# Kernel tuning notes

Hardware: AMD Instinct MI355X
Metric: run time of the kernel (lower is better)

The kernel has to match this reference:

```python
import jax, jax.numpy as jnp
import numpy as np

N_NODES = 50000
N_EDGES = 500000
D_NODE = 64
D_EDGE = 32
MSG_DIM = 2 * D_NODE + D_EDGE      # 160
HID_DIM = MSG_DIM + D_NODE         # 224
ALPHA = 0.01                       # LeakyReLU slope


def setup_inputs() -> dict:
    key = jax.random.key(0)
    ks = jax.random.split(key, 8)
    h_n = jax.random.normal(ks[0], (N_NODES, D_NODE), dtype=jnp.float32)
    h_e = jax.random.normal(ks[1], (N_EDGES, D_EDGE), dtype=jnp.float32)
    src = jax.random.randint(ks[2], (N_EDGES,), 0, N_NODES, dtype=jnp.int32)
    dst = jax.random.randint(ks[3], (N_EDGES,), 0, N_NODES, dtype=jnp.int32)
    W_msg = jax.random.normal(ks[4], (MSG_DIM, MSG_DIM), dtype=jnp.float32) * 0.05
    b_msg = jax.random.normal(ks[5], (MSG_DIM,), dtype=jnp.float32) * 0.05
    W_hid = jax.random.normal(ks[6], (HID_DIM, HID_DIM), dtype=jnp.float32) * 0.05
    b_hid = jax.random.normal(ks[7], (HID_DIM,), dtype=jnp.float32) * 0.05
    return {"h_n": h_n, "h_e": h_e, "src": src, "dst": dst,
            "W_msg": W_msg, "b_msg": b_msg, "W_hid": W_hid, "b_hid": b_hid}


def reference(h_n, h_e, src, dst, W_msg, b_msg, W_hid, b_hid):
    # --- message: gather src/dst node features + edge features, linear + leaky_relu ---
    m_input = jnp.concatenate([h_n[src], h_n[dst], h_e], axis=-1)   # [E, MSG_DIM]
    m = jax.nn.leaky_relu(m_input @ W_msg.T + b_msg, negative_slope=ALPHA)
    # --- reduce: sum messages at destination nodes (DGL fn.sum) ---
    m_sum = jax.ops.segment_sum(m, dst, num_segments=N_NODES)       # [N, MSG_DIM]
    # --- update: concat(m_sum, h_n), linear + leaky_relu ---
    h_input = jnp.concatenate([m_sum, h_n], axis=-1)                # [N, HID_DIM]
    h_out = jax.nn.leaky_relu(h_input @ W_hid.T + b_hid, negative_slope=ALPHA)
    # single graph with unique node ids: split/squeeze is identity
    return h_out
```

## Files before the change

kernel.cpp:

```cpp
#include <hip/hip_runtime.h>

#define N_NODES 50000
#define N_EDGES 500000
#define D_NODE 64
#define D_EDGE 32
#define MSG_DIM 160
#define HID_DIM 224
#define ALPHA 0.01f

#define FNB 16
#define NBKT 3125
#define BKT_CAP 256
#define A_STRIDE 168
#define MT_STRIDE 72
#define CURSOR_PAD 16
#define CVT_BLKS 3200
#define SCAT_BLKS 1954

typedef unsigned short u16;
typedef unsigned long long u64;
typedef short short8 __attribute__((ext_vector_type(8)));
typedef float float4v __attribute__((ext_vector_type(4)));

static __device__ __forceinline__ u16 f2bf(float f) {
    unsigned int u = __float_as_uint(f);
    u += 0x7fffu + ((u >> 16) & 1u);
    return (u16)(u >> 16);
}

__global__ __launch_bounds__(256) void cvt_scatter(const float* __restrict__ h_n,
                                                   const float* __restrict__ W_msg,
                                                   const float* __restrict__ W_hid,
                                                   const int* __restrict__ src,
                                                   const int* __restrict__ dst,
                                                   u16* __restrict__ hn_bf,
                                                   u16* __restrict__ Wm_bf,
                                                   u16* __restrict__ Wh_bf,
                                                   int* __restrict__ cursor,
                                                   u64* __restrict__ pack) {
    const int b = blockIdx.x;
    if (b < CVT_BLKS) {
        int i = b * 256 + threadIdx.x;
        const float* in; u16* outp; int j;
        if (i < 800000)      { in = h_n;   outp = hn_bf; j = i; }
        else if (i < 806400) { in = W_msg; outp = Wm_bf; j = i - 800000; }
        else if (i < 818944) { in = W_hid; outp = Wh_bf; j = i - 806400; }
        else return;
        float4 v = reinterpret_cast<const float4*>(in)[j];
        ushort4 o;
        o.x = f2bf(v.x); o.y = f2bf(v.y); o.z = f2bf(v.z); o.w = f2bf(v.w);
        reinterpret_cast<ushort4*>(outp)[j] = o;
    } else {
        int e = (b - CVT_BLKS) * 256 + threadIdx.x;
        if (e < N_EDGES) {
            int d = dst[e];
            int bk = d >> 4;
            int idx = atomicAdd(&cursor[bk * CURSOR_PAD], 1);
            if (idx < BKT_CAP)
                pack[(size_t)bk * BKT_CAP + idx] =
                    ((u64)e << 34) | ((u64)d << 17) | (u64)src[e];
        }
    }
}

__global__ __launch_bounds__(256) void fused_kernel(
    const u16* __restrict__ hn_bf, const float* __restrict__ h_e,
    const u64* __restrict__ pack, const int* __restrict__ cursor,
    const u16* __restrict__ Wm_bf, const float* __restrict__ b_msg,
    const u16* __restrict__ Wh_bf, const float* __restrict__ b_hid,
    float* __restrict__ out)
{
    __shared__ alignas(16) u16 X_lds[64 * A_STRIDE];
    __shared__ alignas(16) u16 MT[4 * 16 * MT_STRIDE];
    __shared__ alignas(16) u16 dst16[64];

    const int tid = threadIdx.x;
    const int n0 = blockIdx.x * FNB;
    const int p_begin = blockIdx.x * BKT_CAP;
    int ecnt = cursor[blockIdx.x * CURSOR_PAD];
    if (ecnt > BKT_CAP) ecnt = BKT_CAP;
    const int p_end = p_begin + ecnt;

    const int wave = tid >> 6, lane = tid & 63;
    const int qd = lane >> 4, l15 = lane & 15;
    const int e_loc = tid >> 2, j4 = tid & 3;

    const int nchunk = (wave < 2) ? 3 : 2;
    float biasv[3];
#pragma unroll
    for (int ci = 0; ci < 3; ++ci) {
        const int c = wave + ci * 4;
        biasv[ci] = (c < 10) ? b_msg[c * 16 + l15] : 0.f;
    }
    float4v m_acc[3] = {{0,0,0,0},{0,0,0,0},{0,0,0,0}};
    u16* MTw = &MT[wave * 16 * MT_STRIDE];

    u64 pk_cur = 0, pk_nxt = 0;
    uint4 sA, sB, dA, dB;
    float4 heA, heB;
    if (p_begin < p_end) {
        int pp = p_begin + e_loc;
        int pidx = (pp < p_end) ? pp : (p_end - 1);
        pk_cur = pack[pidx];
        const int s  = (int)(pk_cur & 0x1FFFF);
        const int d  = (int)((pk_cur >> 17) & 0x1FFFF);
        const int eo = (int)(pk_cur >> 34);
        const uint4* srow = reinterpret_cast<const uint4*>(hn_bf + (size_t)s * D_NODE);
        const uint4* drow = reinterpret_cast<const uint4*>(hn_bf + (size_t)d * D_NODE);
        sA = srow[j4 * 2]; sB = srow[j4 * 2 + 1];
        dA = drow[j4 * 2]; dB = drow[j4 * 2 + 1];
        const float4* he = reinterpret_cast<const float4*>(h_e + (size_t)eo * D_EDGE);
        heA = he[j4 * 2]; heB = he[j4 * 2 + 1];
        int pp1 = pp + 64;
        pk_nxt = pack[(pp1 < p_end) ? pp1 : (p_end - 1)];
    }

    for (int p0 = p_begin; p0 < p_end; p0 += 64) {
        {
            const bool padE = (p0 + e_loc >= p_end);
            const int d = (int)((pk_cur >> 17) & 0x1FFFF);
            if (j4 == 0) dst16[e_loc] = padE ? (u16)0xFFFFu : (u16)(d - n0);
            uint4* Arow = reinterpret_cast<uint4*>(&X_lds[e_loc * A_STRIDE]);
            Arow[j4 * 2]     = sA;
            Arow[j4 * 2 + 1] = sB;
            Arow[8 + j4 * 2]     = dA;
            Arow[8 + j4 * 2 + 1] = dB;
            ushort4 lo, hi;
            lo.x = f2bf(heA.x); lo.y = f2bf(heA.y); lo.z = f2bf(heA.z); lo.w = f2bf(heA.w);
            hi.x = f2bf(heB.x); hi.y = f2bf(heB.y); hi.z = f2bf(heB.z); hi.w = f2bf(heB.w);
            ushort4* Aus = reinterpret_cast<ushort4*>(Arow);
            Aus[32 + j4 * 2]     = lo;
            Aus[32 + j4 * 2 + 1] = hi;
        }
        __syncthreads();

        short8 xf[4][5];
#pragma unroll
        for (int s = 0; s < 4; ++s)
#pragma unroll
            for (int ks = 0; ks < 5; ++ks)
                xf[s][ks] = *reinterpret_cast<const short8*>(
                    &X_lds[(s * 16 + l15) * A_STRIDE + ks * 32 + qd * 8]);

        short8 a2[2];
#pragma unroll
        for (int fi = 0; fi < 2; ++fi) {
            short8 dv = *reinterpret_cast<const short8*>(&dst16[fi * 32 + qd * 8]);
            short8 t;
#pragma unroll
            for (int j = 0; j < 8; ++j)
                t[j] = (short)(((int)(u16)dv[j] == l15) ? 0x3F80 : 0);
            a2[fi] = t;
        }

        if (p0 + 64 < p_end) {
            pk_cur = pk_nxt;
            const int s  = (int)(pk_cur & 0x1FFFF);
            const int eo = (int)(pk_cur >> 34);
            const int d  = (int)((pk_cur >> 17) & 0x1FFFF);
            const uint4* srow = reinterpret_cast<const uint4*>(hn_bf + (size_t)s * D_NODE);
            const uint4* drow = reinterpret_cast<const uint4*>(hn_bf + (size_t)d * D_NODE);
            sA = srow[j4 * 2]; sB = srow[j4 * 2 + 1];
            dA = drow[j4 * 2]; dB = drow[j4 * 2 + 1];
            const float4* he = reinterpret_cast<const float4*>(h_e + (size_t)eo * D_EDGE);
            heA = he[j4 * 2]; heB = he[j4 * 2 + 1];
            int pp2 = p0 + 128 + e_loc;
            pk_nxt = pack[(pp2 < p_end) ? pp2 : (p_end - 1)];
        }
        __syncthreads();

        for (int ci = 0; ci < nchunk; ++ci) {
            const int c = wave + ci * 4;
            const int fbase = c * 16;
            short8 wf[5];
#pragma unroll
            for (int ks = 0; ks < 5; ++ks)
                wf[ks] = *reinterpret_cast<const short8*>(
                    Wm_bf + (size_t)(fbase + l15) * MSG_DIM + ks * 32 + qd * 8);
            const float bias = biasv[ci];
#pragma unroll
            for (int s = 0; s < 4; ++s) {
                float4v acc = {0.f, 0.f, 0.f, 0.f};
#pragma unroll
                for (int ks = 0; ks < 5; ++ks)
                    acc = __builtin_amdgcn_mfma_f32_16x16x32_bf16(xf[s][ks], wf[ks], acc, 0, 0, 0);
                float v0 = acc[0] + bias, v1 = acc[1] + bias,
                      v2 = acc[2] + bias, v3 = acc[3] + bias;
                v0 = fmaxf(v0, ALPHA * v0); v1 = fmaxf(v1, ALPHA * v1);
                v2 = fmaxf(v2, ALPHA * v2); v3 = fmaxf(v3, ALPHA * v3);
                ushort4 m4;
                m4.x = f2bf(v0); m4.y = f2bf(v1); m4.z = f2bf(v2); m4.w = f2bf(v3);
                *reinterpret_cast<ushort4*>(&MTw[l15 * MT_STRIDE + s * 16 + qd * 4]) = m4;
            }
            short8 b2_0 = *reinterpret_cast<const short8*>(&MTw[l15 * MT_STRIDE + qd * 8]);
            short8 b2_1 = *reinterpret_cast<const short8*>(&MTw[l15 * MT_STRIDE + 32 + qd * 8]);
            m_acc[ci] = __builtin_amdgcn_mfma_f32_16x16x32_bf16(a2[0], b2_0, m_acc[ci], 0, 0, 0);
            m_acc[ci] = __builtin_amdgcn_mfma_f32_16x16x32_bf16(a2[1], b2_1, m_acc[ci], 0, 0, 0);
        }
    }
    __syncthreads();

    u16* Xb = X_lds;
    for (int ci = 0; ci < nchunk; ++ci) {
        const int c = wave + ci * 4;
#pragma unroll
        for (int r = 0; r < 4; ++r)
            Xb[(qd * 4 + r) * A_STRIDE + c * 16 + l15] = f2bf(m_acc[ci][r]);
    }
    __syncthreads();

    const int node = n0 + l15;
    short8 b_frag[7];
#pragma unroll
    for (int ks = 0; ks < 5; ++ks)
        b_frag[ks] = *reinterpret_cast<const short8*>(
            &Xb[l15 * A_STRIDE + ks * 32 + qd * 8]);
#pragma unroll
    for (int ks = 5; ks < 7; ++ks)
        b_frag[ks] = *reinterpret_cast<const short8*>(
            hn_bf + (size_t)node * D_NODE + (ks - 5) * 32 + qd * 8);

    for (int c = wave; c < 14; c += 4) {
        float4v acc = {0.f, 0.f, 0.f, 0.f};
#pragma unroll
        for (int ks = 0; ks < 7; ++ks) {
            short8 a = *reinterpret_cast<const short8*>(
                Wh_bf + (size_t)(c * 16 + l15) * HID_DIM + ks * 32 + qd * 8);
            acc = __builtin_amdgcn_mfma_f32_16x16x32_bf16(a, b_frag[ks], acc, 0, 0, 0);
        }
        const float4 bias = *reinterpret_cast<const float4*>(b_hid + c * 16 + qd * 4);
        float v0 = acc[0] + bias.x, v1 = acc[1] + bias.y,
              v2 = acc[2] + bias.z, v3 = acc[3] + bias.w;
        v0 = fmaxf(v0, ALPHA * v0); v1 = fmaxf(v1, ALPHA * v1);
        v2 = fmaxf(v2, ALPHA * v2); v3 = fmaxf(v3, ALPHA * v3);
        float4 o; o.x = v0; o.y = v1; o.z = v2; o.w = v3;
        *reinterpret_cast<float4*>(&out[(size_t)node * HID_DIM + c * 16 + qd * 4]) = o;
    }
}

extern "C" void kernel_launch(void* const* d_in, const int* in_sizes, int n_in,
                              void* d_out, int out_size, void* d_ws, size_t ws_size,
                              hipStream_t stream)
{
    const float* h_n   = (const float*)d_in[0];
    const float* h_e   = (const float*)d_in[1];
    const int*   src   = (const int*)d_in[2];
    const int*   dst   = (const int*)d_in[3];
    const float* W_msg = (const float*)d_in[4];
    const float* b_msg = (const float*)d_in[5];
    const float* W_hid = (const float*)d_in[6];
    const float* b_hid = (const float*)d_in[7];
    float* out = (float*)d_out;

    char* ws = (char*)d_ws;
    u16* hn_bf  = (u16*)(ws + 0);
    u16* Wm_bf  = (u16*)(ws + 6400000);
    u16* Wh_bf  = (u16*)(ws + 6451200);
    int* cursor = (int*)(ws + 6551552);
    u64* pack   = (u64*)(ws + 6751552);

    hipMemsetAsync(cursor, 0, (size_t)NBKT * CURSOR_PAD * sizeof(int), stream);
    cvt_scatter<<<CVT_BLKS + SCAT_BLKS, 256, 0, stream>>>(
        h_n, W_msg, W_hid, src, dst, hn_bf, Wm_bf, Wh_bf, cursor, pack);
    fused_kernel<<<NBKT, 256, 0, stream>>>(
        hn_bf, h_e, pack, cursor, Wm_bf, b_msg, Wh_bf, b_hid, out);
}
```

Measured before the change: 271.8 us.

## Load MFMA edge fragments directly from global memory, drop LDS staging

```diff
diff --git a/kernel.cpp b/kernel.cpp
--- a/kernel.cpp
+++ b/kernel.cpp
@@ -11,7 +11,7 @@
 #define FNB 16
 #define NBKT 3125
 #define BKT_CAP 256
-#define A_STRIDE 168
+#define XB_STRIDE 168
 #define MT_STRIDE 72
 #define CURSOR_PAD 16
 #define CVT_BLKS 3200
@@ -63,27 +63,25 @@
     }
 }
 
-__global__ __launch_bounds__(256) void fused_kernel(
+__global__ __launch_bounds__(256, 4) void fused_kernel(
     const u16* __restrict__ hn_bf, const float* __restrict__ h_e,
     const u64* __restrict__ pack, const int* __restrict__ cursor,
     const u16* __restrict__ Wm_bf, const float* __restrict__ b_msg,
     const u16* __restrict__ Wh_bf, const float* __restrict__ b_hid,
     float* __restrict__ out)
 {
-    __shared__ alignas(16) u16 X_lds[64 * A_STRIDE];
     __shared__ alignas(16) u16 MT[4 * 16 * MT_STRIDE];
-    __shared__ alignas(16) u16 dst16[64];
+    __shared__ alignas(16) u16 Xb[FNB * XB_STRIDE];
 
     const int tid = threadIdx.x;
     const int n0 = blockIdx.x * FNB;
     const int p_begin = blockIdx.x * BKT_CAP;
     int ecnt = cursor[blockIdx.x * CURSOR_PAD];
     if (ecnt > BKT_CAP) ecnt = BKT_CAP;
-    const int p_end = p_begin + ecnt;
 
     const int wave = tid >> 6, lane = tid & 63;
     const int qd = lane >> 4, l15 = lane & 15;
-    const int e_loc = tid >> 2, j4 = tid & 3;
+    const int myrow = n0 + l15;
 
     const int nchunk = (wave < 2) ? 3 : 2;
     float biasv[3];
@@ -95,79 +93,50 @@
     float4v m_acc[3] = {{0,0,0,0},{0,0,0,0},{0,0,0,0}};
     u16* MTw = &MT[wave * 16 * MT_STRIDE];
 
-    u64 pk_cur = 0, pk_nxt = 0;
-    uint4 sA, sB, dA, dB;
-    float4 heA, heB;
-    if (p_begin < p_end) {
-        int pp = p_begin + e_loc;
-        int pidx = (pp < p_end) ? pp : (p_end - 1);
-        pk_cur = pack[pidx];
-        const int s  = (int)(pk_cur & 0x1FFFF);
-        const int d  = (int)((pk_cur >> 17) & 0x1FFFF);
-        const int eo = (int)(pk_cur >> 34);
-        const uint4* srow = reinterpret_cast<const uint4*>(hn_bf + (size_t)s * D_NODE);
-        const uint4* drow = reinterpret_cast<const uint4*>(hn_bf + (size_t)d * D_NODE);
-        sA = srow[j4 * 2]; sB = srow[j4 * 2 + 1];
-        dA = drow[j4 * 2]; dB = drow[j4 * 2 + 1];
-        const float4* he = reinterpret_cast<const float4*>(h_e + (size_t)eo * D_EDGE);
-        heA = he[j4 * 2]; heB = he[j4 * 2 + 1];
-        int pp1 = pp + 64;
-        pk_nxt = pack[(pp1 < p_end) ? pp1 : (p_end - 1)];
-    }
-
-    for (int p0 = p_begin; p0 < p_end; p0 += 64) {
-        {
-            const bool padE = (p0 + e_loc >= p_end);
-            const int d = (int)((pk_cur >> 17) & 0x1FFFF);
-            if (j4 == 0) dst16[e_loc] = padE ? (u16)0xFFFFu : (u16)(d - n0);
-            uint4* Arow = reinterpret_cast<uint4*>(&X_lds[e_loc * A_STRIDE]);
-            Arow[j4 * 2]     = sA;
-            Arow[j4 * 2 + 1] = sB;
-            Arow[8 + j4 * 2]     = dA;
-            Arow[8 + j4 * 2 + 1] = dB;
-            ushort4 lo, hi;
-            lo.x = f2bf(heA.x); lo.y = f2bf(heA.y); lo.z = f2bf(heA.z); lo.w = f2bf(heA.w);
-            hi.x = f2bf(heB.x); hi.y = f2bf(heB.y); hi.z = f2bf(heB.z); hi.w = f2bf(heB.w);
-            ushort4* Aus = reinterpret_cast<ushort4*>(Arow);
-            Aus[32 + j4 * 2]     = lo;
-            Aus[32 + j4 * 2 + 1] = hi;
-        }
-        __syncthreads();
-
+    for (int p0 = 0; p0 < ecnt; p0 += 64) {
         short8 xf[4][5];
 #pragma unroll
-        for (int s = 0; s < 4; ++s)
-#pragma unroll
-            for (int ks = 0; ks < 5; ++ks)
-                xf[s][ks] = *reinterpret_cast<const short8*>(
-                    &X_lds[(s * 16 + l15) * A_STRIDE + ks * 32 + qd * 8]);
+        for (int s = 0; s < 4; ++s) {
+            int x = p0 + s * 16 + l15;
+            if (x > ecnt - 1) x = ecnt - 1;
+            const u64 pk = pack[p_begin + x];
+            const int sr = (int)(pk & 0x1FFFF);
+            const int dr = (int)((pk >> 17) & 0x1FFFF);
+            const int eo = (int)(pk >> 34);
+            const short8* srow = reinterpret_cast<const short8*>(
+                hn_bf + (size_t)sr * D_NODE + qd * 8);
+            xf[s][0] = srow[0];
+            xf[s][1] = srow[4];
+            const short8* drow = reinterpret_cast<const short8*>(
+                hn_bf + (size_t)dr * D_NODE + qd * 8);
+            xf[s][2] = drow[0];
+            xf[s][3] = drow[4];
+            const float4* he = reinterpret_cast<const float4*>(
+                h_e + (size_t)eo * D_EDGE + qd * 8);
+            float4 ha = he[0], hb = he[1];
+            short8 t;
+            t[0] = (short)f2bf(ha.x); t[1] = (short)f2bf(ha.y);
+            t[2] = (short)f2bf(ha.z); t[3] = (short)f2bf(ha.w);
+            t[4] = (short)f2bf(hb.x); t[5] = (short)f2bf(hb.y);
+            t[6] = (short)f2bf(hb.z); t[7] = (short)f2bf(hb.w);
+            xf[s][4] = t;
+        }
 
         short8 a2[2];
 #pragma unroll
         for (int fi = 0; fi < 2; ++fi) {
-            short8 dv = *reinterpret_cast<const short8*>(&dst16[fi * 32 + qd * 8]);
+            const int xb = p0 + fi * 32 + qd * 8;
+            const u64* pb = pack + p_begin + xb;
+            const int nv = ecnt - xb;
             short8 t;
 #pragma unroll
-            for (int j = 0; j < 8; ++j)
-                t[j] = (short)(((int)(u16)dv[j] == l15) ? 0x3F80 : 0);
+            for (int j = 0; j < 8; ++j) {
+                const u64 pk = pb[j];
+                const int dr = (int)((pk >> 17) & 0x1FFFF);
+                t[j] = (short)((j < nv && dr == myrow) ? 0x3F80 : 0);
+            }
             a2[fi] = t;
         }
-
-        if (p0 + 64 < p_end) {
-            pk_cur = pk_nxt;
-            const int s  = (int)(pk_cur & 0x1FFFF);
-            const int eo = (int)(pk_cur >> 34);
-            const int d  = (int)((pk_cur >> 17) & 0x1FFFF);
-            const uint4* srow = reinterpret_cast<const uint4*>(hn_bf + (size_t)s * D_NODE);
-            const uint4* drow = reinterpret_cast<const uint4*>(hn_bf + (size_t)d * D_NODE);
-            sA = srow[j4 * 2]; sB = srow[j4 * 2 + 1];
-            dA = drow[j4 * 2]; dB = drow[j4 * 2 + 1];
-            const float4* he = reinterpret_cast<const float4*>(h_e + (size_t)eo * D_EDGE);
-            heA = he[j4 * 2]; heB = he[j4 * 2 + 1];
-            int pp2 = p0 + 128 + e_loc;
-            pk_nxt = pack[(pp2 < p_end) ? pp2 : (p_end - 1)];
-        }
-        __syncthreads();
 
         for (int ci = 0; ci < nchunk; ++ci) {
             const int c = wave + ci * 4;
@@ -198,14 +167,12 @@
             m_acc[ci] = __builtin_amdgcn_mfma_f32_16x16x32_bf16(a2[1], b2_1, m_acc[ci], 0, 0, 0);
         }
     }
-    __syncthreads();
-
-    u16* Xb = X_lds;
+
     for (int ci = 0; ci < nchunk; ++ci) {
         const int c = wave + ci * 4;
 #pragma unroll
         for (int r = 0; r < 4; ++r)
-            Xb[(qd * 4 + r) * A_STRIDE + c * 16 + l15] = f2bf(m_acc[ci][r]);
+            Xb[(qd * 4 + r) * XB_STRIDE + c * 16 + l15] = f2bf(m_acc[ci][r]);
     }
     __syncthreads();
 
@@ -214,7 +181,7 @@
 #pragma unroll
     for (int ks = 0; ks < 5; ++ks)
         b_frag[ks] = *reinterpret_cast<const short8*>(
-            &Xb[l15 * A_STRIDE + ks * 32 + qd * 8]);
+            &Xb[l15 * XB_STRIDE + ks * 32 + qd * 8]);
 #pragma unroll
     for (int ks = 5; ks < 7; ++ks)
         b_frag[ks] = *reinterpret_cast<const short8*>(
```

New measurement: 380.9 us. 40.1% more time.

## Merge memset, convert/scatter, and fused compute into one cooperative persistent kernel

Applied to the files above, without the earlier changes.

```diff
diff --git a/kernel.cpp b/kernel.cpp
--- a/kernel.cpp
+++ b/kernel.cpp
@@ -1,4 +1,7 @@
 #include <hip/hip_runtime.h>
+#include <hip/hip_cooperative_groups.h>
+
+namespace cg = cooperative_groups;
 
 #define N_NODES 50000
 #define N_EDGES 500000
@@ -14,8 +17,7 @@
 #define A_STRIDE 168
 #define MT_STRIDE 72
 #define CURSOR_PAD 16
-#define CVT_BLKS 3200
-#define SCAT_BLKS 1954
+#define CVT_N 818944
 
 typedef unsigned short u16;
 typedef unsigned long long u64;
@@ -28,59 +30,47 @@
     return (u16)(u >> 16);
 }
 
-__global__ __launch_bounds__(256) void cvt_scatter(const float* __restrict__ h_n,
-                                                   const float* __restrict__ W_msg,
-                                                   const float* __restrict__ W_hid,
-                                                   const int* __restrict__ src,
-                                                   const int* __restrict__ dst,
-                                                   u16* __restrict__ hn_bf,
-                                                   u16* __restrict__ Wm_bf,
-                                                   u16* __restrict__ Wh_bf,
-                                                   int* __restrict__ cursor,
-                                                   u64* __restrict__ pack) {
-    const int b = blockIdx.x;
-    if (b < CVT_BLKS) {
-        int i = b * 256 + threadIdx.x;
+__global__ __launch_bounds__(256, 4) void mega_kernel(
+    const float* __restrict__ h_n, const float* __restrict__ h_e,
+    const int* __restrict__ src, const int* __restrict__ dst,
+    const float* __restrict__ W_msg, const float* __restrict__ b_msg,
+    const float* __restrict__ W_hid, const float* __restrict__ b_hid,
+    u16* __restrict__ hn_bf, u16* __restrict__ Wm_bf, u16* __restrict__ Wh_bf,
+    int* __restrict__ cursor, u64* __restrict__ pack,
+    float* __restrict__ out)
+{
+    cg::grid_group grid = cg::this_grid();
+    const int tid  = threadIdx.x;
+    const int gtid = blockIdx.x * 256 + tid;
+    const int gstr = gridDim.x * 256;
+
+    for (int i = gtid; i < NBKT * CURSOR_PAD; i += gstr) cursor[i] = 0;
+    grid.sync();
+
+    for (int i = gtid; i < CVT_N; i += gstr) {
         const float* in; u16* outp; int j;
         if (i < 800000)      { in = h_n;   outp = hn_bf; j = i; }
         else if (i < 806400) { in = W_msg; outp = Wm_bf; j = i - 800000; }
-        else if (i < 818944) { in = W_hid; outp = Wh_bf; j = i - 806400; }
-        else return;
+        else                 { in = W_hid; outp = Wh_bf; j = i - 806400; }
         float4 v = reinterpret_cast<const float4*>(in)[j];
         ushort4 o;
         o.x = f2bf(v.x); o.y = f2bf(v.y); o.z = f2bf(v.z); o.w = f2bf(v.w);
         reinterpret_cast<ushort4*>(outp)[j] = o;
-    } else {
-        int e = (b - CVT_BLKS) * 256 + threadIdx.x;
-        if (e < N_EDGES) {
-            int d = dst[e];
-            int bk = d >> 4;
-            int idx = atomicAdd(&cursor[bk * CURSOR_PAD], 1);
-            if (idx < BKT_CAP)
-                pack[(size_t)bk * BKT_CAP + idx] =
-                    ((u64)e << 34) | ((u64)d << 17) | (u64)src[e];
-        }
-    }
-}
-
-__global__ __launch_bounds__(256) void fused_kernel(
-    const u16* __restrict__ hn_bf, const float* __restrict__ h_e,
-    const u64* __restrict__ pack, const int* __restrict__ cursor,
-    const u16* __restrict__ Wm_bf, const float* __restrict__ b_msg,
-    const u16* __restrict__ Wh_bf, const float* __restrict__ b_hid,
-    float* __restrict__ out)
-{
+    }
+    for (int e = gtid; e < N_EDGES; e += gstr) {
+        int d = dst[e];
+        int bk = d >> 4;
+        int idx = atomicAdd(&cursor[bk * CURSOR_PAD], 1);
+        if (idx < BKT_CAP)
+            pack[(size_t)bk * BKT_CAP + idx] =
+                ((u64)e << 34) | ((u64)d << 17) | (u64)src[e];
+    }
+    grid.sync();
+
     __shared__ alignas(16) u16 X_lds[64 * A_STRIDE];
     __shared__ alignas(16) u16 MT[4 * 16 * MT_STRIDE];
     __shared__ alignas(16) u16 dst16[64];
 
-    const int tid = threadIdx.x;
-    const int n0 = blockIdx.x * FNB;
-    const int p_begin = blockIdx.x * BKT_CAP;
-    int ecnt = cursor[blockIdx.x * CURSOR_PAD];
-    if (ecnt > BKT_CAP) ecnt = BKT_CAP;
-    const int p_end = p_begin + ecnt;
-
     const int wave = tid >> 6, lane = tid & 63;
     const int qd = lane >> 4, l15 = lane & 15;
     const int e_loc = tid >> 2, j4 = tid & 3;
@@ -92,149 +82,159 @@
         const int c = wave + ci * 4;
         biasv[ci] = (c < 10) ? b_msg[c * 16 + l15] : 0.f;
     }
-    float4v m_acc[3] = {{0,0,0,0},{0,0,0,0},{0,0,0,0}};
     u16* MTw = &MT[wave * 16 * MT_STRIDE];
 
-    u64 pk_cur = 0, pk_nxt = 0;
-    uint4 sA, sB, dA, dB;
-    float4 heA, heB;
-    if (p_begin < p_end) {
-        int pp = p_begin + e_loc;
-        int pidx = (pp < p_end) ? pp : (p_end - 1);
-        pk_cur = pack[pidx];
-        const int s  = (int)(pk_cur & 0x1FFFF);
-        const int d  = (int)((pk_cur >> 17) & 0x1FFFF);
-        const int eo = (int)(pk_cur >> 34);
-        const uint4* srow = reinterpret_cast<const uint4*>(hn_bf + (size_t)s * D_NODE);
-        const uint4* drow = reinterpret_cast<const uint4*>(hn_bf + (size_t)d * D_NODE);
-        sA = srow[j4 * 2]; sB = srow[j4 * 2 + 1];
-        dA = drow[j4 * 2]; dB = drow[j4 * 2 + 1];
-        const float4* he = reinterpret_cast<const float4*>(h_e + (size_t)eo * D_EDGE);
-        heA = he[j4 * 2]; heB = he[j4 * 2 + 1];
-        int pp1 = pp + 64;
-        pk_nxt = pack[(pp1 < p_end) ? pp1 : (p_end - 1)];
-    }
-
-    for (int p0 = p_begin; p0 < p_end; p0 += 64) {
-        {
-            const bool padE = (p0 + e_loc >= p_end);
-            const int d = (int)((pk_cur >> 17) & 0x1FFFF);
-            if (j4 == 0) dst16[e_loc] = padE ? (u16)0xFFFFu : (u16)(d - n0);
-            uint4* Arow = reinterpret_cast<uint4*>(&X_lds[e_loc * A_STRIDE]);
-            Arow[j4 * 2]     = sA;
-            Arow[j4 * 2 + 1] = sB;
-            Arow[8 + j4 * 2]     = dA;
-            Arow[8 + j4 * 2 + 1] = dB;
-            ushort4 lo, hi;
-            lo.x = f2bf(heA.x); lo.y = f2bf(heA.y); lo.z = f2bf(heA.z); lo.w = f2bf(heA.w);
-            hi.x = f2bf(heB.x); hi.y = f2bf(heB.y); hi.z = f2bf(heB.z); hi.w = f2bf(heB.w);
-            ushort4* Aus = reinterpret_cast<ushort4*>(Arow);
-            Aus[32 + j4 * 2]     = lo;
-            Aus[32 + j4 * 2 + 1] = hi;
-        }
-        __syncthreads();
-
-        short8 xf[4][5];
-#pragma unroll
-        for (int s = 0; s < 4; ++s)
-#pragma unroll
-            for (int ks = 0; ks < 5; ++ks)
-                xf[s][ks] = *reinterpret_cast<const short8*>(
-                    &X_lds[(s * 16 + l15) * A_STRIDE + ks * 32 + qd * 8]);
-
-        short8 a2[2];
-#pragma unroll
-        for (int fi = 0; fi < 2; ++fi) {
-            short8 dv = *reinterpret_cast<const short8*>(&dst16[fi * 32 + qd * 8]);
-            short8 t;
-#pragma unroll
-            for (int j = 0; j < 8; ++j)
-                t[j] = (short)(((int)(u16)dv[j] == l15) ? 0x3F80 : 0);
-            a2[fi] = t;
-        }
-
-        if (p0 + 64 < p_end) {
-            pk_cur = pk_nxt;
+    for (int bk = blockIdx.x; bk < NBKT; bk += gridDim.x) {
+        const int n0 = bk * FNB;
+        const int p_begin = bk * BKT_CAP;
+        int ecnt = cursor[bk * CURSOR_PAD];
+        if (ecnt > BKT_CAP) ecnt = BKT_CAP;
+        const int p_end = p_begin + ecnt;
+
+        float4v m_acc[3] = {{0,0,0,0},{0,0,0,0},{0,0,0,0}};
+
+        u64 pk_cur = 0, pk_nxt = 0;
+        uint4 sA, sB, dA, dB;
+        float4 heA, heB;
+        if (p_begin < p_end) {
+            int pp = p_begin + e_loc;
+            int pidx = (pp < p_end) ? pp : (p_end - 1);
+            pk_cur = pack[pidx];
             const int s  = (int)(pk_cur & 0x1FFFF);
+            const int d  = (int)((pk_cur >> 17) & 0x1FFFF);
             const int eo = (int)(pk_cur >> 34);
-            const int d  = (int)((pk_cur >> 17) & 0x1FFFF);
             const uint4* srow = reinterpret_cast<const uint4*>(hn_bf + (size_t)s * D_NODE);
             const uint4* drow = reinterpret_cast<const uint4*>(hn_bf + (size_t)d * D_NODE);
             sA = srow[j4 * 2]; sB = srow[j4 * 2 + 1];
             dA = drow[j4 * 2]; dB = drow[j4 * 2 + 1];
             const float4* he = reinterpret_cast<const float4*>(h_e + (size_t)eo * D_EDGE);
             heA = he[j4 * 2]; heB = he[j4 * 2 + 1];
-            int pp2 = p0 + 128 + e_loc;
-            pk_nxt = pack[(pp2 < p_end) ? pp2 : (p_end - 1)];
+            int pp1 = pp + 64;
+            pk_nxt = pack[(pp1 < p_end) ? pp1 : (p_end - 1)];
+        }
+
+        for (int p0 = p_begin; p0 < p_end; p0 += 64) {
+            {
+                const bool padE = (p0 + e_loc >= p_end);
+                const int d = (int)((pk_cur >> 17) & 0x1FFFF);
+                if (j4 == 0) dst16[e_loc] = padE ? (u16)0xFFFFu : (u16)(d - n0);
+                uint4* Arow = reinterpret_cast<uint4*>(&X_lds[e_loc * A_STRIDE]);
+                Arow[j4 * 2]     = sA;
+                Arow[j4 * 2 + 1] = sB;
+                Arow[8 + j4 * 2]     = dA;
+                Arow[8 + j4 * 2 + 1] = dB;
+                ushort4 lo, hi;
+                lo.x = f2bf(heA.x); lo.y = f2bf(heA.y); lo.z = f2bf(heA.z); lo.w = f2bf(heA.w);
+                hi.x = f2bf(heB.x); hi.y = f2bf(heB.y); hi.z = f2bf(heB.z); hi.w = f2bf(heB.w);
+                ushort4* Aus = reinterpret_cast<ushort4*>(Arow);
+                Aus[32 + j4 * 2]     = lo;
+                Aus[32 + j4 * 2 + 1] = hi;
+            }
+            __syncthreads();
+
+            short8 xf[4][5];
+#pragma unroll
+            for (int s = 0; s < 4; ++s)
+#pragma unroll
+                for (int ks = 0; ks < 5; ++ks)
+                    xf[s][ks] = *reinterpret_cast<const short8*>(
+                        &X_lds[(s * 16 + l15) * A_STRIDE + ks * 32 + qd * 8]);
+
+            short8 a2[2];
+#pragma unroll
+            for (int fi = 0; fi < 2; ++fi) {
+                short8 dv = *reinterpret_cast<const short8*>(&dst16[fi * 32 + qd * 8]);
+                short8 t;
+#pragma unroll
+                for (int j = 0; j < 8; ++j)
+                    t[j] = (short)(((int)(u16)dv[j] == l15) ? 0x3F80 : 0);
+                a2[fi] = t;
+            }
+
+            if (p0 + 64 < p_end) {
+                pk_cur = pk_nxt;
+                const int s  = (int)(pk_cur & 0x1FFFF);
+                const int eo = (int)(pk_cur >> 34);
+                const uint4* srow = reinterpret_cast<const uint4*>(hn_bf + (size_t)s * D_NODE);
+                const uint4* drow = reinterpret_cast<const uint4*>(
+                    hn_bf + (size_t)((pk_cur >> 17) & 0x1FFFF) * D_NODE);
+                sA = srow[j4 * 2]; sB = srow[j4 * 2 + 1];
+                dA = drow[j4 * 2]; dB = drow[j4 * 2 + 1];
+                const float4* he = reinterpret_cast<const float4*>(h_e + (size_t)eo * D_EDGE);
+                heA = he[j4 * 2]; heB = he[j4 * 2 + 1];
+                int pp2 = p0 + 128 + e_loc;
+                pk_nxt = pack[(pp2 < p_end) ? pp2 : (p_end - 1)];
+            }
+            __syncthreads();
+
+            for (int ci = 0; ci < nchunk; ++ci) {
+                const int c = wave + ci * 4;
+                const int fbase = c * 16;
+                short8 wf[5];
+#pragma unroll
+                for (int ks = 0; ks < 5; ++ks)
+                    wf[ks] = *reinterpret_cast<const short8*>(
+                        Wm_bf + (size_t)(fbase + l15) * MSG_DIM + ks * 32 + qd * 8);
+                const float bias = biasv[ci];
+#pragma unroll
+                for (int s = 0; s < 4; ++s) {
+                    float4v acc = {0.f, 0.f, 0.f, 0.f};
+#pragma unroll
+                    for (int ks = 0; ks < 5; ++ks)
+                        acc = __builtin_amdgcn_mfma_f32_16x16x32_bf16(xf[s][ks], wf[ks], acc, 0, 0, 0);
+                    float v0 = acc[0] + bias, v1 = acc[1] + bias,
+                          v2 = acc[2] + bias, v3 = acc[3] + bias;
+                    v0 = fmaxf(v0, ALPHA * v0); v1 = fmaxf(v1, ALPHA * v1);
+                    v2 = fmaxf(v2, ALPHA * v2); v3 = fmaxf(v3, ALPHA * v3);
+                    ushort4 m4;
+                    m4.x = f2bf(v0); m4.y = f2bf(v1); m4.z = f2bf(v2); m4.w = f2bf(v3);
+                    *reinterpret_cast<ushort4*>(&MTw[l15 * MT_STRIDE + s * 16 + qd * 4]) = m4;
+                }
+                short8 b2_0 = *reinterpret_cast<const short8*>(&MTw[l15 * MT_STRIDE + qd * 8]);
+                short8 b2_1 = *reinterpret_cast<const short8*>(&MTw[l15 * MT_STRIDE + 32 + qd * 8]);
+                m_acc[ci] = __builtin_amdgcn_mfma_f32_16x16x32_bf16(a2[0], b2_0, m_acc[ci], 0, 0, 0);
+                m_acc[ci] = __builtin_amdgcn_mfma_f32_16x16x32_bf16(a2[1], b2_1, m_acc[ci], 0, 0, 0);
+            }
         }
         __syncthreads();
 
+        u16* Xb = X_lds;
         for (int ci = 0; ci < nchunk; ++ci) {
             const int c = wave + ci * 4;
-            const int fbase = c * 16;
-            short8 wf[5];
-#pragma unroll
-            for (int ks = 0; ks < 5; ++ks)
-                wf[ks] = *reinterpret_cast<const short8*>(
-                    Wm_bf + (size_t)(fbase + l15) * MSG_DIM + ks * 32 + qd * 8);
-            const float bias = biasv[ci];
-#pragma unroll
-            for (int s = 0; s < 4; ++s) {
-                float4v acc = {0.f, 0.f, 0.f, 0.f};
-#pragma unroll
-                for (int ks = 0; ks < 5; ++ks)
-                    acc = __builtin_amdgcn_mfma_f32_16x16x32_bf16(xf[s][ks], wf[ks], acc, 0, 0, 0);
-                float v0 = acc[0] + bias, v1 = acc[1] + bias,
-                      v2 = acc[2] + bias, v3 = acc[3] + bias;
-                v0 = fmaxf(v0, ALPHA * v0); v1 = fmaxf(v1, ALPHA * v1);
-                v2 = fmaxf(v2, ALPHA * v2); v3 = fmaxf(v3, ALPHA * v3);
-                ushort4 m4;
-                m4.x = f2bf(v0); m4.y = f2bf(v1); m4.z = f2bf(v2); m4.w = f2bf(v3);
-                *reinterpret_cast<ushort4*>(&MTw[l15 * MT_STRIDE + s * 16 + qd * 4]) = m4;
-            }
-            short8 b2_0 = *reinterpret_cast<const short8*>(&MTw[l15 * MT_STRIDE + qd * 8]);
-            short8 b2_1 = *reinterpret_cast<const short8*>(&MTw[l15 * MT_STRIDE + 32 + qd * 8]);
-            m_acc[ci] = __builtin_amdgcn_mfma_f32_16x16x32_bf16(a2[0], b2_0, m_acc[ci], 0, 0, 0);
-            m_acc[ci] = __builtin_amdgcn_mfma_f32_16x16x32_bf16(a2[1], b2_1, m_acc[ci], 0, 0, 0);
-        }
-    }
-    __syncthreads();
-
-    u16* Xb = X_lds;
-    for (int ci = 0; ci < nchunk; ++ci) {
-        const int c = wave + ci * 4;
-#pragma unroll
-        for (int r = 0; r < 4; ++r)
-            Xb[(qd * 4 + r) * A_STRIDE + c * 16 + l15] = f2bf(m_acc[ci][r]);
-    }
-    __syncthreads();
-
-    const int node = n0 + l15;
-    short8 b_frag[7];
-#pragma unroll
-    for (int ks = 0; ks < 5; ++ks)
-        b_frag[ks] = *reinterpret_cast<const short8*>(
-            &Xb[l15 * A_STRIDE + ks * 32 + qd * 8]);
-#pragma unroll
-    for (int ks = 5; ks < 7; ++ks)
-        b_frag[ks] = *reinterpret_cast<const short8*>(
-            hn_bf + (size_t)node * D_NODE + (ks - 5) * 32 + qd * 8);
-
-    for (int c = wave; c < 14; c += 4) {
-        float4v acc = {0.f, 0.f, 0.f, 0.f};
-#pragma unroll
-        for (int ks = 0; ks < 7; ++ks) {
-            short8 a = *reinterpret_cast<const short8*>(
-                Wh_bf + (size_t)(c * 16 + l15) * HID_DIM + ks * 32 + qd * 8);
-            acc = __builtin_amdgcn_mfma_f32_16x16x32_bf16(a, b_frag[ks], acc, 0, 0, 0);
-        }
-        const float4 bias = *reinterpret_cast<const float4*>(b_hid + c * 16 + qd * 4);
-        float v0 = acc[0] + bias.x, v1 = acc[1] + bias.y,
-              v2 = acc[2] + bias.z, v3 = acc[3] + bias.w;
-        v0 = fmaxf(v0, ALPHA * v0); v1 = fmaxf(v1, ALPHA * v1);
-        v2 = fmaxf(v2, ALPHA * v2); v3 = fmaxf(v3, ALPHA * v3);
-        float4 o; o.x = v0; o.y = v1; o.z = v2; o.w = v3;
-        *reinterpret_cast<float4*>(&out[(size_t)node * HID_DIM + c * 16 + qd * 4]) = o;
+#pragma unroll
+            for (int r = 0; r < 4; ++r)
+                Xb[(qd * 4 + r) * A_STRIDE + c * 16 + l15] = f2bf(m_acc[ci][r]);
+        }
+        __syncthreads();
+
+        const int node = n0 + l15;
+        short8 b_frag[7];
+#pragma unroll
+        for (int ks = 0; ks < 5; ++ks)
+            b_frag[ks] = *reinterpret_cast<const short8*>(
+                &Xb[l15 * A_STRIDE + ks * 32 + qd * 8]);
+#pragma unroll
+        for (int ks = 5; ks < 7; ++ks)
+            b_frag[ks] = *reinterpret_cast<const short8*>(
+                hn_bf + (size_t)node * D_NODE + (ks - 5) * 32 + qd * 8);
+
+        for (int c = wave; c < 14; c += 4) {
+            float4v acc = {0.f, 0.f, 0.f, 0.f};
+#pragma unroll
+            for (int ks = 0; ks < 7; ++ks) {
+                short8 a = *reinterpret_cast<const short8*>(
+                    Wh_bf + (size_t)(c * 16 + l15) * HID_DIM + ks * 32 + qd * 8);
+                acc = __builtin_amdgcn_mfma_f32_16x16x32_bf16(a, b_frag[ks], acc, 0, 0, 0);
+            }
+            const float4 bias = *reinterpret_cast<const float4*>(b_hid + c * 16 + qd * 4);
+            float v0 = acc[0] + bias.x, v1 = acc[1] + bias.y,
+                  v2 = acc[2] + bias.z, v3 = acc[3] + bias.w;
+            v0 = fmaxf(v0, ALPHA * v0); v1 = fmaxf(v1, ALPHA * v1);
+            v2 = fmaxf(v2, ALPHA * v2); v3 = fmaxf(v3, ALPHA * v3);
+            float4 o; o.x = v0; o.y = v1; o.z = v2; o.w = v3;
+            *reinterpret_cast<float4*>(&out[(size_t)node * HID_DIM + c * 16 + qd * 4]) = o;
+        }
+        __syncthreads();
     }
 }
 
@@ -259,9 +259,26 @@
     int* cursor = (int*)(ws + 6551552);
     u64* pack   = (u64*)(ws + 6751552);
 
-    hipMemsetAsync(cursor, 0, (size_t)NBKT * CURSOR_PAD * sizeof(int), stream);
-    cvt_scatter<<<CVT_BLKS + SCAT_BLKS, 256, 0, stream>>>(
-        h_n, W_msg, W_hid, src, dst, hn_bf, Wm_bf, Wh_bf, cursor, pack);
-    fused_kernel<<<NBKT, 256, 0, stream>>>(
-        hn_bf, h_e, pack, cursor, Wm_bf, b_msg, Wh_bf, b_hid, out);
+    static int grid_blocks = 0;
+    if (grid_blocks == 0) {
+        int nb = 0;
+        hipOccupancyMaxActiveBlocksPerMultiprocessor(&nb, mega_kernel, 256, 0);
+        if (nb < 1) nb = 1;
+        int dev = 0;
+        hipGetDevice(&dev);
+        hipDeviceProp_t prop;
+        int ncu = 256;
+        if (hipGetDeviceProperties(&prop, dev) == hipSuccess &&
+            prop.multiProcessorCount > 0)
+            ncu = prop.multiProcessorCount;
+        grid_blocks = nb * ncu;
+        if (grid_blocks > NBKT) grid_blocks = NBKT;
+    }
+
+    void* args[] = { (void*)&h_n, (void*)&h_e, (void*)&src, (void*)&dst,
+                     (void*)&W_msg, (void*)&b_msg, (void*)&W_hid, (void*)&b_hid,
+                     (void*)&hn_bf, (void*)&Wm_bf, (void*)&Wh_bf,
+                     (void*)&cursor, (void*)&pack, (void*)&out };
+    hipLaunchCooperativeKernel(mega_kernel, dim3(grid_blocks), dim3(256),
+                               args, 0, stream);
 }
```

Result: slower. 669.9 us (+146.4%).

## Double nodes per block to 32 and drop register prefetch of edge gathers

Applied to the files above, without the earlier changes.

```diff
diff --git a/kernel.cpp b/kernel.cpp
--- a/kernel.cpp
+++ b/kernel.cpp
@@ -8,9 +8,9 @@
 #define HID_DIM 224
 #define ALPHA 0.01f
 
-#define FNB 16
-#define NBKT 3125
-#define BKT_CAP 256
+#define FNB 32
+#define NBKT 1563
+#define BKT_CAP 512
 #define A_STRIDE 168
 #define MT_STRIDE 72
 #define CURSOR_PAD 16
@@ -54,7 +54,7 @@
         int e = (b - CVT_BLKS) * 256 + threadIdx.x;
         if (e < N_EDGES) {
             int d = dst[e];
-            int bk = d >> 4;
+            int bk = d >> 5;
             int idx = atomicAdd(&cursor[bk * CURSOR_PAD], 1);
             if (idx < BKT_CAP)
                 pack[(size_t)bk * BKT_CAP + idx] =
@@ -85,49 +85,41 @@
     const int qd = lane >> 4, l15 = lane & 15;
     const int e_loc = tid >> 2, j4 = tid & 3;
 
-    const int nchunk = (wave < 2) ? 3 : 2;
     float biasv[3];
 #pragma unroll
     for (int ci = 0; ci < 3; ++ci) {
         const int c = wave + ci * 4;
         biasv[ci] = (c < 10) ? b_msg[c * 16 + l15] : 0.f;
     }
-    float4v m_acc[3] = {{0,0,0,0},{0,0,0,0},{0,0,0,0}};
+    float4v m_acc[3][2];
+#pragma unroll
+    for (int ci = 0; ci < 3; ++ci) {
+        m_acc[ci][0] = (float4v){0.f, 0.f, 0.f, 0.f};
+        m_acc[ci][1] = (float4v){0.f, 0.f, 0.f, 0.f};
+    }
     u16* MTw = &MT[wave * 16 * MT_STRIDE];
-
-    u64 pk_cur = 0, pk_nxt = 0;
-    uint4 sA, sB, dA, dB;
-    float4 heA, heB;
-    if (p_begin < p_end) {
-        int pp = p_begin + e_loc;
-        int pidx = (pp < p_end) ? pp : (p_end - 1);
-        pk_cur = pack[pidx];
-        const int s  = (int)(pk_cur & 0x1FFFF);
-        const int d  = (int)((pk_cur >> 17) & 0x1FFFF);
-        const int eo = (int)(pk_cur >> 34);
-        const uint4* srow = reinterpret_cast<const uint4*>(hn_bf + (size_t)s * D_NODE);
-        const uint4* drow = reinterpret_cast<const uint4*>(hn_bf + (size_t)d * D_NODE);
-        sA = srow[j4 * 2]; sB = srow[j4 * 2 + 1];
-        dA = drow[j4 * 2]; dB = drow[j4 * 2 + 1];
-        const float4* he = reinterpret_cast<const float4*>(h_e + (size_t)eo * D_EDGE);
-        heA = he[j4 * 2]; heB = he[j4 * 2 + 1];
-        int pp1 = pp + 64;
-        pk_nxt = pack[(pp1 < p_end) ? pp1 : (p_end - 1)];
-    }
 
     for (int p0 = p_begin; p0 < p_end; p0 += 64) {
         {
-            const bool padE = (p0 + e_loc >= p_end);
-            const int d = (int)((pk_cur >> 17) & 0x1FFFF);
+            int pp = p0 + e_loc;
+            const bool padE = (pp >= p_end); if (padE) pp = p_end - 1;
+            const u64 pk = pack[pp];
+            const int s  = (int)(pk & 0x1FFFF);
+            const int d  = (int)((pk >> 17) & 0x1FFFF);
+            const int eo = (int)(pk >> 34);
             if (j4 == 0) dst16[e_loc] = padE ? (u16)0xFFFFu : (u16)(d - n0);
+            const uint4* srow = reinterpret_cast<const uint4*>(hn_bf + (size_t)s * D_NODE);
+            const uint4* drow = reinterpret_cast<const uint4*>(hn_bf + (size_t)d * D_NODE);
             uint4* Arow = reinterpret_cast<uint4*>(&X_lds[e_loc * A_STRIDE]);
-            Arow[j4 * 2]     = sA;
-            Arow[j4 * 2 + 1] = sB;
-            Arow[8 + j4 * 2]     = dA;
-            Arow[8 + j4 * 2 + 1] = dB;
+            Arow[j4 * 2]     = srow[j4 * 2];
+            Arow[j4 * 2 + 1] = srow[j4 * 2 + 1];
+            Arow[8 + j4 * 2]     = drow[j4 * 2];
+            Arow[8 + j4 * 2 + 1] = drow[j4 * 2 + 1];
+            const float4* he = reinterpret_cast<const float4*>(h_e + (size_t)eo * D_EDGE);
+            float4 p = he[j4 * 2], q = he[j4 * 2 + 1];
             ushort4 lo, hi;
-            lo.x = f2bf(heA.x); lo.y = f2bf(heA.y); lo.z = f2bf(heA.z); lo.w = f2bf(heA.w);
-            hi.x = f2bf(heB.x); hi.y = f2bf(heB.y); hi.z = f2bf(heB.z); hi.w = f2bf(heB.w);
+            lo.x = f2bf(p.x); lo.y = f2bf(p.y); lo.z = f2bf(p.z); lo.w = f2bf(p.w);
+            hi.x = f2bf(q.x); hi.y = f2bf(q.y); hi.z = f2bf(q.z); hi.w = f2bf(q.w);
             ushort4* Aus = reinterpret_cast<ushort4*>(Arow);
             Aus[32 + j4 * 2]     = lo;
             Aus[32 + j4 * 2 + 1] = hi;
@@ -142,35 +134,26 @@
                 xf[s][ks] = *reinterpret_cast<const short8*>(
                     &X_lds[(s * 16 + l15) * A_STRIDE + ks * 32 + qd * 8]);
 
-        short8 a2[2];
+        short8 a2[2][2];
 #pragma unroll
         for (int fi = 0; fi < 2; ++fi) {
             short8 dv = *reinterpret_cast<const short8*>(&dst16[fi * 32 + qd * 8]);
-            short8 t;
-#pragma unroll
-            for (int j = 0; j < 8; ++j)
-                t[j] = (short)(((int)(u16)dv[j] == l15) ? 0x3F80 : 0);
-            a2[fi] = t;
-        }
-
-        if (p0 + 64 < p_end) {
-            pk_cur = pk_nxt;
-            const int s  = (int)(pk_cur & 0x1FFFF);
-            const int eo = (int)(pk_cur >> 34);
-            const int d  = (int)((pk_cur >> 17) & 0x1FFFF);
-            const uint4* srow = reinterpret_cast<const uint4*>(hn_bf + (size_t)s * D_NODE);
-            const uint4* drow = reinterpret_cast<const uint4*>(hn_bf + (size_t)d * D_NODE);
-            sA = srow[j4 * 2]; sB = srow[j4 * 2 + 1];
-            dA = drow[j4 * 2]; dB = drow[j4 * 2 + 1];
-            const float4* he = reinterpret_cast<const float4*>(h_e + (size_t)eo * D_EDGE);
-            heA = he[j4 * 2]; heB = he[j4 * 2 + 1];
-            int pp2 = p0 + 128 + e_loc;
-            pk_nxt = pack[(pp2 < p_end) ? pp2 : (p_end - 1)];
+#pragma unroll
+            for (int h = 0; h < 2; ++h) {
+                const int want = h * 16 + l15;
+                short8 t;
+#pragma unroll
+                for (int j = 0; j < 8; ++j)
+                    t[j] = (short)(((int)(u16)dv[j] == want) ? 0x3F80 : 0);
+                a2[fi][h] = t;
+            }
         }
         __syncthreads();
 
-        for (int ci = 0; ci < nchunk; ++ci) {
+#pragma unroll
+        for (int ci = 0; ci < 3; ++ci) {
             const int c = wave + ci * 4;
+            if (c >= 10) break;
             const int fbase = c * 16;
             short8 wf[5];
 #pragma unroll
@@ -194,47 +177,60 @@
             }
             short8 b2_0 = *reinterpret_cast<const short8*>(&MTw[l15 * MT_STRIDE + qd * 8]);
             short8 b2_1 = *reinterpret_cast<const short8*>(&MTw[l15 * MT_STRIDE + 32 + qd * 8]);
-            m_acc[ci] = __builtin_amdgcn_mfma_f32_16x16x32_bf16(a2[0], b2_0, m_acc[ci], 0, 0, 0);
-            m_acc[ci] = __builtin_amdgcn_mfma_f32_16x16x32_bf16(a2[1], b2_1, m_acc[ci], 0, 0, 0);
+            m_acc[ci][0] = __builtin_amdgcn_mfma_f32_16x16x32_bf16(a2[0][0], b2_0, m_acc[ci][0], 0, 0, 0);
+            m_acc[ci][0] = __builtin_amdgcn_mfma_f32_16x16x32_bf16(a2[1][0], b2_1, m_acc[ci][0], 0, 0, 0);
+            m_acc[ci][1] = __builtin_amdgcn_mfma_f32_16x16x32_bf16(a2[0][1], b2_0, m_acc[ci][1], 0, 0, 0);
+            m_acc[ci][1] = __builtin_amdgcn_mfma_f32_16x16x32_bf16(a2[1][1], b2_1, m_acc[ci][1], 0, 0, 0);
         }
     }
     __syncthreads();
 
     u16* Xb = X_lds;
-    for (int ci = 0; ci < nchunk; ++ci) {
+#pragma unroll
+    for (int ci = 0; ci < 3; ++ci) {
         const int c = wave + ci * 4;
-#pragma unroll
-        for (int r = 0; r < 4; ++r)
-            Xb[(qd * 4 + r) * A_STRIDE + c * 16 + l15] = f2bf(m_acc[ci][r]);
+        if (c >= 10) break;
+#pragma unroll
+        for (int h = 0; h < 2; ++h)
+#pragma unroll
+            for (int r = 0; r < 4; ++r)
+                Xb[(h * 16 + qd * 4 + r) * A_STRIDE + c * 16 + l15] =
+                    f2bf(m_acc[ci][h][r]);
     }
     __syncthreads();
 
-    const int node = n0 + l15;
-    short8 b_frag[7];
-#pragma unroll
-    for (int ks = 0; ks < 5; ++ks)
-        b_frag[ks] = *reinterpret_cast<const short8*>(
-            &Xb[l15 * A_STRIDE + ks * 32 + qd * 8]);
-#pragma unroll
-    for (int ks = 5; ks < 7; ++ks)
-        b_frag[ks] = *reinterpret_cast<const short8*>(
-            hn_bf + (size_t)node * D_NODE + (ks - 5) * 32 + qd * 8);
-
-    for (int c = wave; c < 14; c += 4) {
-        float4v acc = {0.f, 0.f, 0.f, 0.f};
-#pragma unroll
-        for (int ks = 0; ks < 7; ++ks) {
-            short8 a = *reinterpret_cast<const short8*>(
-                Wh_bf + (size_t)(c * 16 + l15) * HID_DIM + ks * 32 + qd * 8);
-            acc = __builtin_amdgcn_mfma_f32_16x16x32_bf16(a, b_frag[ks], acc, 0, 0, 0);
-        }
-        const float4 bias = *reinterpret_cast<const float4*>(b_hid + c * 16 + qd * 4);
-        float v0 = acc[0] + bias.x, v1 = acc[1] + bias.y,
-              v2 = acc[2] + bias.z, v3 = acc[3] + bias.w;
-        v0 = fmaxf(v0, ALPHA * v0); v1 = fmaxf(v1, ALPHA * v1);
-        v2 = fmaxf(v2, ALPHA * v2); v3 = fmaxf(v3, ALPHA * v3);
-        float4 o; o.x = v0; o.y = v1; o.z = v2; o.w = v3;
-        *reinterpret_cast<float4*>(&out[(size_t)node * HID_DIM + c * 16 + qd * 4]) = o;
+#pragma unroll
+    for (int h = 0; h < 2; ++h) {
+        const int node = n0 + h * 16 + l15;
+        const int rnode = (node < N_NODES) ? node : (N_NODES - 1);
+        short8 b_frag[7];
+#pragma unroll
+        for (int ks = 0; ks < 5; ++ks)
+            b_frag[ks] = *reinterpret_cast<const short8*>(
+                &Xb[(h * 16 + l15) * A_STRIDE + ks * 32 + qd * 8]);
+#pragma unroll
+        for (int ks = 5; ks < 7; ++ks)
+            b_frag[ks] = *reinterpret_cast<const short8*>(
+                hn_bf + (size_t)rnode * D_NODE + (ks - 5) * 32 + qd * 8);
+
+        for (int c = wave; c < 14; c += 4) {
+            float4v acc = {0.f, 0.f, 0.f, 0.f};
+#pragma unroll
+            for (int ks = 0; ks < 7; ++ks) {
+                short8 a = *reinterpret_cast<const short8*>(
+                    Wh_bf + (size_t)(c * 16 + l15) * HID_DIM + ks * 32 + qd * 8);
+                acc = __builtin_amdgcn_mfma_f32_16x16x32_bf16(a, b_frag[ks], acc, 0, 0, 0);
+            }
+            const float4 bias = *reinterpret_cast<const float4*>(b_hid + c * 16 + qd * 4);
+            float v0 = acc[0] + bias.x, v1 = acc[1] + bias.y,
+                  v2 = acc[2] + bias.z, v3 = acc[3] + bias.w;
+            v0 = fmaxf(v0, ALPHA * v0); v1 = fmaxf(v1, ALPHA * v1);
+            v2 = fmaxf(v2, ALPHA * v2); v3 = fmaxf(v3, ALPHA * v3);
+            float4 o; o.x = v0; o.y = v1; o.z = v2; o.w = v3;
+            if (node < N_NODES)
+                *reinterpret_cast<float4*>(
+                    &out[(size_t)node * HID_DIM + c * 16 + qd * 4]) = o;
+        }
     }
 }
 
@@ -257,7 +253,7 @@
     u16* Wm_bf  = (u16*)(ws + 6400000);
     u16* Wh_bf  = (u16*)(ws + 6451200);
     int* cursor = (int*)(ws + 6551552);
-    u64* pack   = (u64*)(ws + 6751552);
+    u64* pack   = (u64*)(ws + 6651584);
 
     hipMemsetAsync(cursor, 0, (size_t)NBKT * CURSOR_PAD * sizeof(int), stream);
     cvt_scatter<<<CVT_BLKS + SCAT_BLKS, 256, 0, stream>>>(
```

Result: slower. 284.7 us (+4.7%).
